# Performance work log

Measured on AMD Instinct MI355X. Metric: run time of the kernel, lower is better.

The kernel has to match this reference:

```python
import jax, jax.numpy as jnp
import numpy as np
from jax import lax

HEADS = 6      # n_splits // head_ratio
DHEAD = 64     # hidden // n_splits
ALLH = HEADS * DHEAD  # 384
KS = 9         # conv_kernel_size
PAD = (KS - 1) // 2


def setup_inputs() -> dict:
    key = jax.random.key(0)
    ks = jax.random.split(key, 12)
    B, S, H = 8, 1024, 768
    f = jnp.float32
    return {
        "Q": jax.random.normal(ks[0], (B, S, H), f),
        "K": jax.random.normal(ks[1], (B, S, H), f),
        "V": jax.random.normal(ks[2], (B, S, H), f),
        "Wq": jax.random.normal(ks[3], (H, ALLH), f) * 0.02,
        "Wk": jax.random.normal(ks[4], (H, ALLH), f) * 0.02,
        "Wv": jax.random.normal(ks[5], (H, ALLH), f) * 0.02,
        "dw": jax.random.normal(ks[6], (H, KS), f) * 0.02,        # depthwise conv [C,k]
        "pw": jax.random.normal(ks[7], (ALLH, H), f) * 0.02,      # pointwise conv [out,in]
        "sep_bias": jnp.zeros((ALLH,), f),
        "Wck": jax.random.normal(ks[8], (ALLH, HEADS * KS), f) * 0.02,
        "bck": jnp.zeros((HEADS * KS,), f),
        "Wco": jax.random.normal(ks[9], (H, ALLH), f) * 0.02,
        "bco": jnp.zeros((ALLH,), f),
        "gammas": jnp.zeros((HEADS, 1, 1), f),
        "mask": jnp.ones((B, S), jnp.int32),
    }


def _forward(Q, K, V, Wq, Wk, Wv, dw, pw, sep_bias, Wck, bck, Wco, bco, gammas, mask):
    B, S, H = Q.shape
    q = Q @ Wq  # [B,S,ALLH]
    k = K @ Wk
    v = V @ Wv
    # SeparableConv1D on K: depthwise 'same' conv (groups=H) then 1x1 pointwise + bias
    x = K.transpose(0, 2, 1)  # [B,H,S]
    x = lax.conv_general_dilated(x, dw[:, None, :], (1,), [(PAD, PAD)],
                                 dimension_numbers=("NCH", "OIH", "NCH"),
                                 feature_group_count=H)
    keyconv = jnp.einsum("bcs,oc->bso", x, pw) + sep_bias  # [B,S,ALLH]
    # span-dynamic-conv kernel weights, softmax over kernel taps
    conv_attn = keyconv * q
    kern = (conv_attn @ Wck + bck).reshape(B, S, HEADS, KS)
    kern = jax.nn.softmax(kern, axis=-1)
    # unfold V-projection into local windows and apply per-position kernels
    co = V @ Wco + bco                                   # [B,S,ALLH]
    cop = jnp.pad(co, ((0, 0), (PAD, PAD), (0, 0)))
    win = jnp.stack([cop[:, j:j + S, :] for j in range(KS)], axis=-1)  # [B,S,ALLH,KS]
    win = win.reshape(B, S, HEADS, DHEAD, KS)
    conv_out = jnp.einsum("bshdk,bshk->bshd", win, kern)  # [B,S,HEADS,DHEAD]
    # standard attention scores
    q4 = q.reshape(B, S, HEADS, DHEAD).transpose(0, 2, 1, 3)
    k4 = k.reshape(B, S, HEADS, DHEAD).transpose(0, 2, 1, 3)
    v4 = v.reshape(B, S, HEADS, DHEAD).transpose(0, 2, 1, 3)
    scores = jnp.einsum("bhid,bhjd->bhij", q4, k4) / jnp.sqrt(jnp.float32(DHEAD))
    m = (mask != 0)[:, None, None, :]  # key mask [B,1,1,S]
    # monotonic distance scores (no-grad in original -> stop_gradient)
    sc = lax.stop_gradient(scores)
    p_ = jax.nn.softmax(jnp.where(m, sc, -1e32), axis=-1) * m.astype(sc.dtype)
    cum = jnp.cumsum(p_, axis=-1)
    tot = jnp.sum(p_, axis=-1, keepdims=True)
    idx = jnp.arange(S)
    pos = jnp.abs(idx[None, :] - idx[:, None]).astype(jnp.float32)  # |i-j|
    dist = jnp.sqrt(jnp.clip((tot - cum) * pos, 0.0))
    gamma = -jax.nn.softplus(gammas)[None]  # [1,HEADS,1,1]
    effect = jnp.clip(jnp.exp(dist * gamma), 1e-5, 1e5)
    scores2 = jnp.where(m, scores * effect, -1e8)
    probs = jax.nn.softmax(scores2, axis=-1)  # dropout_p=0 -> identity
    ctx = jnp.einsum("bhij,bhjd->bihd", probs, v4)  # [B,S,HEADS,DHEAD]
    out = jnp.concatenate([ctx, conv_out], axis=2).reshape(B, S, 2 * ALLH)
    return out


def reference(Q, K, V, Wq, Wk, Wv, dw, pw, sep_bias, Wck, bck, Wco, bco, gammas, mask):
    return _forward(Q, K, V, Wq, Wk, Wv, dw, pw, sep_bias, Wck, bck, Wco, bco, gammas, mask)
```

## Files before the change

kernel.cpp:

```cpp
#include <hip/hip_runtime.h>
#include <math.h>

#define BATCH 8
#define SEQ   1024
#define HID   768
#define HEADS 6
#define DHEAD 64
#define ALLH  384
#define KS    9
#define PADC  4
#define MROWS (BATCH*SEQ)

typedef __attribute__((ext_vector_type(8))) short bf16x8;
typedef __attribute__((ext_vector_type(4))) short bf16x4;
typedef __attribute__((ext_vector_type(4))) float f32x4;

__device__ __forceinline__ ushort f2bf(float x) {
    unsigned u = __float_as_uint(x);
    unsigned r = (u + 0x7FFFu + ((u >> 16) & 1u)) >> 16;
    return (ushort)r;
}
__device__ __forceinline__ unsigned pk2(float a, float b) {
    return (unsigned)f2bf(a) | ((unsigned)f2bf(b) << 16);
}
__device__ __forceinline__ float fexp2(float x) {
#if __has_builtin(__builtin_amdgcn_exp2f)
    return __builtin_amdgcn_exp2f(x);
#else
    return exp2f(x);
#endif
}
__device__ __forceinline__ float fsqrt(float x) {
#if __has_builtin(__builtin_amdgcn_sqrtf)
    return __builtin_amdgcn_sqrtf(x);
#else
    return __sqrtf(x);
#endif
}
__device__ __forceinline__ unsigned cvtpk(float a, float b) {
    unsigned r; asm("v_cvt_pk_bf16_f32 %0, %1, %2" : "=v"(r) : "v"(a), "v"(b)); return r;
}

__device__ __forceinline__ void mfma16(f32x4& c4, bf16x4 a, bf16x4 b) {
#if __has_builtin(__builtin_amdgcn_mfma_f32_16x16x16bf16_1k)
    c4 = __builtin_amdgcn_mfma_f32_16x16x16bf16_1k(a, b, c4, 0, 0, 0);
#else
    asm volatile("v_mfma_f32_16x16x16_bf16 %0, %1, %2, %0" : "+v"(c4) : "v"(a), "v"(b));
#endif
}

__global__ __launch_bounds__(256) void dconv_kernel(const float* __restrict__ Kin,
                                                    const float* __restrict__ dw,
                                                    ushort* __restrict__ y) {
    const int t = threadIdx.x;
    const int c4l = t & 63;
    const int sg = t >> 6;
    const int c4 = blockIdx.x * 64 + c4l;
    const int s0 = blockIdx.y * 64 + sg * 16;
    const int b = blockIdx.z;
    const int c = c4 * 4;

    const float* base = Kin + (size_t)b * SEQ * HID + c;
    ushort* ybase = y + (size_t)b * SEQ * HID + c;

    float wv[4][KS];
#pragma unroll
    for (int j = 0; j < 4; ++j)
#pragma unroll
        for (int tt = 0; tt < KS; ++tt) wv[j][tt] = dw[(c + j) * KS + tt];

    float4 win[KS];
#pragma unroll
    for (int tt = 0; tt < KS; ++tt) {
        int sj = s0 - PADC + tt;
        win[tt] = (sj >= 0 && sj < SEQ) ? *reinterpret_cast<const float4*>(base + (size_t)sj * HID)
                                        : float4{0.f, 0.f, 0.f, 0.f};
    }

#pragma unroll
    for (int i = 0; i < 16; ++i) {
        const int s = s0 + i;
        float4 acc = {0.f, 0.f, 0.f, 0.f};
#pragma unroll
        for (int tt = 0; tt < KS; ++tt) {
            acc.x += win[tt].x * wv[0][tt];
            acc.y += win[tt].y * wv[1][tt];
            acc.z += win[tt].z * wv[2][tt];
            acc.w += win[tt].w * wv[3][tt];
        }
        uint2 o;
        o.x = pk2(acc.x, acc.y); o.y = pk2(acc.z, acc.w);
        *reinterpret_cast<uint2*>(ybase + (size_t)s * HID) = o;
#pragma unroll
        for (int tt = 0; tt < KS - 1; ++tt) win[tt] = win[tt + 1];
        int sj = s + 1 + PADC;
        win[KS - 1] = (sj < SEQ) ? *reinterpret_cast<const float4*>(base + (size_t)sj * HID)
                                 : float4{0.f, 0.f, 0.f, 0.f};
    }
}

__global__ __launch_bounds__(256) void wcvt_kernel(const float* __restrict__ W0, const float* __restrict__ W1,
                                                   const float* __restrict__ W2, const float* __restrict__ W3,
                                                   ushort* __restrict__ O0, ushort* __restrict__ O1,
                                                   ushort* __restrict__ O2, ushort* __restrict__ O3) {
    __shared__ float t[32][33];
    int wsel = blockIdx.z;
    const float* W = wsel == 0 ? W0 : wsel == 1 ? W1 : wsel == 2 ? W2 : W3;
    ushort* O = wsel == 0 ? O0 : wsel == 1 ? O1 : wsel == 2 ? O2 : O3;
    int kt = blockIdx.x * 32;
    int nt = blockIdx.y * 32;
    int tx = threadIdx.x & 31, ty = threadIdx.x >> 5;
#pragma unroll
    for (int i = 0; i < 4; ++i)
        t[ty + i * 8][tx] = W[(size_t)(kt + ty + i * 8) * ALLH + nt + tx];
    __syncthreads();
#pragma unroll
    for (int i = 0; i < 4; ++i)
        O[(size_t)(nt + ty + i * 8) * HID + kt + tx] = f2bf(t[tx][ty + i * 8]);
}

__global__ __launch_bounds__(256) void pwcvt_kernel(const float* __restrict__ pw, ushort* __restrict__ pwb) {
    int i = blockIdx.x * 256 + threadIdx.x;
    if (i < ALLH * HID) pwb[i] = f2bf(pw[i]);
}

template <int BMODE, bool HAS_BIAS, bool AF32>
__global__ __launch_bounds__(256) void gemm_mfma(const void* __restrict__ Ap,
                                                 const ushort* __restrict__ Bt,
                                                 const float* __restrict__ bias,
                                                 float* __restrict__ C,
                                                 ushort* __restrict__ Chm) {
    __shared__ __align__(16) ushort As[64 * 64];
    __shared__ __align__(16) ushort Bs[64 * 64];

    const int bid = blockIdx.x;
    const int swz = (bid & 7) * 96 + (bid >> 3);
    const int n0 = (swz % 6) * 64;
    const int m0 = (swz / 6) * 64;

    const int tid = threadIdx.x;
    const int lane = tid & 63;
    const int w = tid >> 6;
    const int g = lane >> 4;
    const int c = lane & 15;

    const ushort* Ab = (const ushort*)Ap;
    const float* Af = (const float*)Ap;

    f32x4 acc[4] = {{0,0,0,0},{0,0,0,0},{0,0,0,0},{0,0,0,0}};

    for (int k0 = 0; k0 < HID; k0 += 64) {
        __syncthreads();
#pragma unroll
        for (int it = 0; it < 2; ++it) {
            int e = tid + it * 256;
            int row = e >> 3;
            int c8 = (e & 7) * 8;
            int boff = row * 128 + ((c8 * 2) ^ ((row & 7) << 4));
            if (AF32) {
                const float4 f0 = *reinterpret_cast<const float4*>(&Af[(size_t)(m0 + row) * HID + k0 + c8]);
                const float4 f1 = *reinterpret_cast<const float4*>(&Af[(size_t)(m0 + row) * HID + k0 + c8 + 4]);
                uint4 p;
                p.x = pk2(f0.x, f0.y); p.y = pk2(f0.z, f0.w);
                p.z = pk2(f1.x, f1.y); p.w = pk2(f1.z, f1.w);
                *reinterpret_cast<uint4*>((char*)As + boff) = p;
            } else {
                const uint4 av = *reinterpret_cast<const uint4*>(&Ab[(size_t)(m0 + row) * HID + k0 + c8]);
                *reinterpret_cast<uint4*>((char*)As + boff) = av;
            }
            const uint4 bv = *reinterpret_cast<const uint4*>(&Bt[(size_t)(n0 + row) * HID + k0 + c8]);
            *reinterpret_cast<uint4*>((char*)Bs + boff) = bv;
        }
        __syncthreads();

        const int arow = w * 16 + c;
        const int asw = (arow & 7) << 4;
        bf16x8 af0 = *reinterpret_cast<const bf16x8*>((char*)As + arow * 128 + ((g * 16) ^ asw));
        bf16x8 af1 = *reinterpret_cast<const bf16x8*>((char*)As + arow * 128 + ((64 + g * 16) ^ asw));
#pragma unroll
        for (int nq = 0; nq < 4; ++nq) {
            const int brow = nq * 16 + c;
            const int bsw = (brow & 7) << 4;
            bf16x8 bf0 = *reinterpret_cast<const bf16x8*>((char*)Bs + brow * 128 + ((g * 16) ^ bsw));
            bf16x8 bf1 = *reinterpret_cast<const bf16x8*>((char*)Bs + brow * 128 + ((64 + g * 16) ^ bsw));
            acc[nq] = __builtin_amdgcn_mfma_f32_16x16x32_bf16(af0, bf0, acc[nq], 0, 0, 0);
            acc[nq] = __builtin_amdgcn_mfma_f32_16x16x32_bf16(af1, bf1, acc[nq], 0, 0, 0);
        }
    }

#pragma unroll
    for (int nq = 0; nq < 4; ++nq) {
        const int n = n0 + nq * 16 + c;
        const float bv = HAS_BIAS ? bias[n] : 0.f;
#pragma unroll
        for (int r = 0; r < 4; ++r) {
            const int m = m0 + w * 16 + g * 4 + r;
            float v = acc[nq][r] + bv;
            if (BMODE == 0 || BMODE == 1) C[(size_t)m * ALLH + n] = v;
            if (BMODE == 1) {
                int bb = m >> 10, s = m & 1023;
                int head = n >> 6, d = n & 63;
                Chm[(((size_t)bb * HEADS + head) * SEQ + s) * 64 + d] = f2bf(v);
            }
            if (BMODE == 2) {
                int bb = m >> 10, s = m & 1023;
                int head = n >> 6, d = n & 63;
                char* tb = (char*)Chm + (((size_t)(bb * HEADS + head) * 16 + (s >> 6)) * 4096) * 2;
                unsigned off = (unsigned)(s & 63) * 128 + (((unsigned)(d * 2)) ^ ((s & 7) << 4));
                *reinterpret_cast<ushort*>(tb + off) = f2bf(v);
            }
        }
    }
}

__global__ __launch_bounds__(256) void gemm_vv(const float* __restrict__ Af,
                                               const ushort* __restrict__ B1t,
                                               const ushort* __restrict__ B2t,
                                               const float* __restrict__ bco,
                                               ushort* __restrict__ vhm,
                                               float* __restrict__ cob) {
    __shared__ __align__(16) ushort As[64 * 64];
    __shared__ __align__(16) ushort B1s[64 * 64];
    __shared__ __align__(16) ushort B2s[64 * 64];

    const int bid = blockIdx.x;
    const int swz = (bid & 7) * 96 + (bid >> 3);
    const int n0 = (swz % 6) * 64;
    const int m0 = (swz / 6) * 64;

    const int tid = threadIdx.x;
    const int lane = tid & 63;
    const int w = tid >> 6;
    const int g = lane >> 4;
    const int c = lane & 15;

    f32x4 acc1[4] = {{0,0,0,0},{0,0,0,0},{0,0,0,0},{0,0,0,0}};
    f32x4 acc2[4] = {{0,0,0,0},{0,0,0,0},{0,0,0,0},{0,0,0,0}};

    for (int k0 = 0; k0 < HID; k0 += 64) {
        __syncthreads();
#pragma unroll
        for (int it = 0; it < 2; ++it) {
            int e = tid + it * 256;
            int row = e >> 3;
            int c8 = (e & 7) * 8;
            int boff = row * 128 + ((c8 * 2) ^ ((row & 7) << 4));
            const float4 f0 = *reinterpret_cast<const float4*>(&Af[(size_t)(m0 + row) * HID + k0 + c8]);
            const float4 f1 = *reinterpret_cast<const float4*>(&Af[(size_t)(m0 + row) * HID + k0 + c8 + 4]);
            uint4 p;
            p.x = pk2(f0.x, f0.y); p.y = pk2(f0.z, f0.w);
            p.z = pk2(f1.x, f1.y); p.w = pk2(f1.z, f1.w);
            *reinterpret_cast<uint4*>((char*)As + boff) = p;
            const uint4 b1v = *reinterpret_cast<const uint4*>(&B1t[(size_t)(n0 + row) * HID + k0 + c8]);
            *reinterpret_cast<uint4*>((char*)B1s + boff) = b1v;
            const uint4 b2v = *reinterpret_cast<const uint4*>(&B2t[(size_t)(n0 + row) * HID + k0 + c8]);
            *reinterpret_cast<uint4*>((char*)B2s + boff) = b2v;
        }
        __syncthreads();

        const int arow = w * 16 + c;
        const int asw = (arow & 7) << 4;
        bf16x8 af0 = *reinterpret_cast<const bf16x8*>((char*)As + arow * 128 + ((g * 16) ^ asw));
        bf16x8 af1 = *reinterpret_cast<const bf16x8*>((char*)As + arow * 128 + ((64 + g * 16) ^ asw));
#pragma unroll
        for (int nq = 0; nq < 4; ++nq) {
            const int brow = nq * 16 + c;
            const int bsw = (brow & 7) << 4;
            bf16x8 v10 = *reinterpret_cast<const bf16x8*>((char*)B1s + brow * 128 + ((g * 16) ^ bsw));
            bf16x8 v11 = *reinterpret_cast<const bf16x8*>((char*)B1s + brow * 128 + ((64 + g * 16) ^ bsw));
            acc1[nq] = __builtin_amdgcn_mfma_f32_16x16x32_bf16(af0, v10, acc1[nq], 0, 0, 0);
            acc1[nq] = __builtin_amdgcn_mfma_f32_16x16x32_bf16(af1, v11, acc1[nq], 0, 0, 0);
            bf16x8 v20 = *reinterpret_cast<const bf16x8*>((char*)B2s + brow * 128 + ((g * 16) ^ bsw));
            bf16x8 v21 = *reinterpret_cast<const bf16x8*>((char*)B2s + brow * 128 + ((64 + g * 16) ^ bsw));
            acc2[nq] = __builtin_amdgcn_mfma_f32_16x16x32_bf16(af0, v20, acc2[nq], 0, 0, 0);
            acc2[nq] = __builtin_amdgcn_mfma_f32_16x16x32_bf16(af1, v21, acc2[nq], 0, 0, 0);
        }
    }

    {
        const int head = n0 >> 6;
        const int bb = m0 >> 10;
        const int st = (m0 & 1023) >> 6;
        char* tb = (char*)vhm + (((size_t)(bb * HEADS + head) * 16 + st) * 4096) * 2;
#pragma unroll
        for (int nq = 0; nq < 4; ++nq) {
            const int d = nq * 16 + c;
            unsigned off = (unsigned)d * 128 + (((unsigned)(32 * w + 8 * g)) ^ ((d & 7) << 4));
            uint2 vv;
            vv.x = pk2(acc1[nq][0], acc1[nq][1]);
            vv.y = pk2(acc1[nq][2], acc1[nq][3]);
            *reinterpret_cast<uint2*>(tb + off) = vv;
        }
    }
#pragma unroll
    for (int nq = 0; nq < 4; ++nq) {
        const int n = n0 + nq * 16 + c;
        const float bv = bco[n];
#pragma unroll
        for (int r = 0; r < 4; ++r) {
            const int m = m0 + w * 16 + g * 4 + r;
            cob[(size_t)m * ALLH + n] = acc2[nq][r] + bv;
        }
    }
}

__global__ __launch_bounds__(256) void spankern_kernel(const float* __restrict__ keyconv,
                                                       const float* __restrict__ q,
                                                       const float* __restrict__ Wck,
                                                       const float* __restrict__ bck,
                                                       float* __restrict__ kern_sm) {
    __shared__ float ca[4][ALLH];
    __shared__ float kv[4][64];
    int row0 = blockIdx.x * 4;
    int tid = threadIdx.x;
    int r = tid >> 6;
    int lane = tid & 63;
    int row = row0 + r;
    for (int e = lane; e < ALLH; e += 64) {
        size_t off = (size_t)row * ALLH + e;
        ca[r][e] = keyconv[off] * q[off];
    }
    __syncthreads();
    float val = 0.f;
    if (lane < HEADS * KS) {
        for (int kidx = 0; kidx < ALLH; ++kidx)
            val += ca[r][kidx] * Wck[kidx * (HEADS * KS) + lane];
        val += bck[lane];
    }
    kv[r][lane] = val;
    __syncthreads();
    if (lane < HEADS) {
        float mx = -INFINITY;
#pragma unroll
        for (int t = 0; t < KS; ++t) mx = fmaxf(mx, kv[r][lane * KS + t]);
        float e[KS];
        float sum = 0.f;
#pragma unroll
        for (int t = 0; t < KS; ++t) {
            e[t] = expf(kv[r][lane * KS + t] - mx);
            sum += e[t];
        }
        float inv = 1.f / sum;
#pragma unroll
        for (int t = 0; t < KS; ++t)
            kern_sm[((size_t)row * HEADS + lane) * KS + t] = e[t] * inv;
    }
}

__global__ __launch_bounds__(256) void convout_kernel(const float* __restrict__ co,
                                                      const float* __restrict__ kern_sm,
                                                      float* __restrict__ out) {
    int idx = blockIdx.x * 256 + threadIdx.x;
    if (idx >= MROWS * (ALLH / 4)) return;
    int c4 = idx % (ALLH / 4);
    int s = (idx / (ALLH / 4)) % SEQ;
    int b = idx / ((ALLH / 4) * SEQ);
    int c = c4 * 4;
    int h = c >> 6;
    const float* ks = &kern_sm[(((size_t)b * SEQ + s) * HEADS + h) * KS];
    float kt[KS];
#pragma unroll
    for (int t = 0; t < KS; ++t) kt[t] = ks[t];
    float4 acc = {0.f, 0.f, 0.f, 0.f};
#pragma unroll
    for (int t = 0; t < KS; ++t) {
        int sj = s + t - PADC;
        if (sj >= 0 && sj < SEQ) {
            const float4 cv = *reinterpret_cast<const float4*>(&co[((size_t)b * SEQ + sj) * ALLH + c]);
            acc.x += cv.x * kt[t];
            acc.y += cv.y * kt[t];
            acc.z += cv.z * kt[t];
            acc.w += cv.w * kt[t];
        }
    }
    *reinterpret_cast<float4*>(&out[((size_t)b * SEQ + s) * (2 * ALLH) + ALLH + c]) = acc;
}

__global__ __launch_bounds__(256) void attn_mfma(const ushort* __restrict__ qh,
                                                 const ushort* __restrict__ kh,
                                                 const ushort* __restrict__ vh,
                                                 const int* __restrict__ mask,
                                                 const float* __restrict__ gammas,
                                                 float* __restrict__ out) {
    __shared__ __align__(16) ushort kbuf[64 * 64];
    __shared__ __align__(16) ushort vbuf[64 * 64];
    __shared__ float s_msk[SEQ];

    const int bid = blockIdx.x;
    const int blk = (bid & 7) * 96 + (bid >> 3);
    const int qt = blk & 15;
    const int h = (blk >> 4) % HEADS;
    const int b = blk / (16 * HEADS);
    const int i0 = qt * 64;
    const int tid = threadIdx.x;
    const int lane = tid & 63;
    const int w = tid >> 6;
    const int g = lane >> 4;
    const int c = lane & 15;

    const float LOG2E = 1.44269504f;
    float g0 = gammas[h];
    float gamma2 = -(fmaxf(g0, 0.f) + log1pf(expf(-fabsf(g0)))) * LOG2E;
    const float SLOG2 = 0.125f * LOG2E;

    const ushort* ktiles = kh + ((size_t)(b * HEADS + h) * 16) * 4096;
    const ushort* vtiles = vh + ((size_t)(b * HEADS + h) * 16) * 4096;
    const ushort* qhb = qh + ((size_t)b * HEADS + h) * SEQ * 64;

    for (int e = tid; e < SEQ; e += 256)
        s_msk[e] = (mask[b * SEQ + e] != 0) ? 1.f : 0.f;

    bf16x8 qf0, qf1;
    {
        const ushort* qrow = qhb + (size_t)(i0 + w * 16 + c) * 64 + g * 8;
        qf0 = *reinterpret_cast<const bf16x8*>(qrow);
        qf1 = *reinterpret_cast<const bf16x8*>(qrow + 32);
    }

    float Tacc = 0.f;
    for (int chk = 0; chk < 16; ++chk) {
        __syncthreads();
        const ushort* ktp = ktiles + chk * 4096;
#pragma unroll
        for (int it = 0; it < 2; ++it) {
            int e16 = (tid + it * 256) * 16;
            *reinterpret_cast<uint4*>((char*)kbuf + e16) =
                *reinterpret_cast<const uint4*>((const char*)ktp + e16);
        }
        __syncthreads();
        const int j0 = chk * 64;
#pragma unroll
        for (int m = 0; m < 4; ++m) {
            f32x4 acc = {0.f, 0.f, 0.f, 0.f};
            int row = m * 16 + c;
            int sw = (row & 7) << 4;
            bf16x8 kf0 = *reinterpret_cast<const bf16x8*>((char*)kbuf + row * 128 + ((g * 16) ^ sw));
            bf16x8 kf1 = *reinterpret_cast<const bf16x8*>((char*)kbuf + row * 128 + ((64 + g * 16) ^ sw));
            acc = __builtin_amdgcn_mfma_f32_16x16x32_bf16(kf0, qf0, acc, 0, 0, 0);
            acc = __builtin_amdgcn_mfma_f32_16x16x32_bf16(kf1, qf1, acc, 0, 0, 0);
#pragma unroll
            for (int r = 0; r < 4; ++r) {
                float mk = s_msk[j0 + m * 16 + g * 4 + r];
                Tacc += mk * fexp2(acc[r] * SLOG2);
            }
        }
    }
    Tacc += __shfl_xor(Tacc, 16, 64);
    Tacc += __shfl_xor(Tacc, 32, 64);
    const float T = Tacc;
    const float invT = (T > 0.f) ? 1.f / T : 0.f;

    f32x4 ctx0 = {0,0,0,0}, ctx1 = {0,0,0,0}, ctx2 = {0,0,0,0}, ctx3 = {0,0,0,0};
    float l2acc = 0.f;
    float base = 0.f;
    const float iq = (float)(i0 + w * 16 + c);
    const unsigned vx = (unsigned)((c & 7) << 4);

    for (int chk = 0; chk < 16; ++chk) {
        __syncthreads();
        const ushort* ktp = ktiles + chk * 4096;
        const ushort* vtp = vtiles + chk * 4096;
#pragma unroll
        for (int it = 0; it < 2; ++it) {
            int e16 = (tid + it * 256) * 16;
            *reinterpret_cast<uint4*>((char*)kbuf + e16) =
                *reinterpret_cast<const uint4*>((const char*)ktp + e16);
            *reinterpret_cast<uint4*>((char*)vbuf + e16) =
                *reinterpret_cast<const uint4*>((const char*)vtp + e16);
        }
        __syncthreads();
        const int j0 = chk * 64;
#pragma unroll
        for (int m = 0; m < 4; ++m) {
            f32x4 acc = {0.f, 0.f, 0.f, 0.f};
            int row = m * 16 + c;
            int sw = (row & 7) << 4;
            bf16x8 kf0 = *reinterpret_cast<const bf16x8*>((char*)kbuf + row * 128 + ((g * 16) ^ sw));
            bf16x8 kf1 = *reinterpret_cast<const bf16x8*>((char*)kbuf + row * 128 + ((64 + g * 16) ^ sw));
            acc = __builtin_amdgcn_mfma_f32_16x16x32_bf16(kf0, qf0, acc, 0, 0, 0);
            acc = __builtin_amdgcn_mfma_f32_16x16x32_bf16(kf1, qf1, acc, 0, 0, 0);

            float sl[4], mk[4], incl[4];
            float li = 0.f;
#pragma unroll
            for (int r = 0; r < 4; ++r) {
                mk[r] = s_msk[j0 + m * 16 + g * 4 + r];
                sl[r] = acc[r] * SLOG2;
                float e = mk[r] * fexp2(sl[r]);
                li += e;
                incl[r] = li;
            }
            float gs = li;
            float up = __shfl_up(gs, 16, 64); if (g >= 1) gs += up;
            up = __shfl_up(gs, 32, 64); if (g >= 2) gs += up;
            float gexcl = gs - li;
            float ttot = __shfl(gs, 48 + c, 64);

            const float dbase = iq - (float)(j0 + m * 16 + g * 4);
            float p2[4];
#pragma unroll
            for (int r = 0; r < 4; ++r) {
                float cum = base + gexcl + incl[r];
                float rem = fmaxf(1.0f - cum * invT, 0.f);
                float pos = fabsf(dbase - (float)r);
                float dist = fsqrt(rem * pos);
                float eff = fmaxf(fexp2(dist * gamma2), 1e-5f);
                p2[r] = mk[r] * fexp2(sl[r] * eff);
                l2acc += p2[r];
            }
            base += ttot;

            union { uint2 u; bf16x4 v; } pu;
            pu.u.x = cvtpk(p2[0], p2[1]);
            pu.u.y = cvtpk(p2[2], p2[3]);
            bf16x4 pa = pu.v;

            const unsigned cb = ((unsigned)(32 * m + 8 * g)) ^ vx;
#pragma unroll
            for (int t = 0; t < 4; ++t) {
                bf16x4 vfrag = *reinterpret_cast<const bf16x4*>((char*)vbuf + (unsigned)(c + 16 * t) * 128 + cb);
                if (t == 0) mfma16(ctx0, pa, vfrag);
                else if (t == 1) mfma16(ctx1, pa, vfrag);
                else if (t == 2) mfma16(ctx2, pa, vfrag);
                else mfma16(ctx3, pa, vfrag);
            }
        }
    }
    l2acc += __shfl_xor(l2acc, 16, 64);
    l2acc += __shfl_xor(l2acc, 32, 64);
    const float invl2 = 1.f / l2acc;

#pragma unroll
    for (int r = 0; r < 4; ++r) {
        float inv_r = __shfl(invl2, g * 4 + r, 64);
        int qrow = i0 + w * 16 + g * 4 + r;
        float* orow = out + ((size_t)b * SEQ + qrow) * (2 * ALLH) + h * DHEAD;
        orow[c +  0] = ctx0[r] * inv_r;
        orow[c + 16] = ctx1[r] * inv_r;
        orow[c + 32] = ctx2[r] * inv_r;
        orow[c + 48] = ctx3[r] * inv_r;
    }
}

extern "C" void kernel_launch(void* const* d_in, const int* in_sizes, int n_in,
                              void* d_out, int out_size, void* d_ws, size_t ws_size,
                              hipStream_t stream) {
    const float* Q = (const float*)d_in[0];
    const float* Kin = (const float*)d_in[1];
    const float* V = (const float*)d_in[2];
    const float* Wq = (const float*)d_in[3];
    const float* Wk = (const float*)d_in[4];
    const float* Wv = (const float*)d_in[5];
    const float* dw = (const float*)d_in[6];
    const float* pw = (const float*)d_in[7];
    const float* sep_bias = (const float*)d_in[8];
    const float* Wck = (const float*)d_in[9];
    const float* bck = (const float*)d_in[10];
    const float* Wco = (const float*)d_in[11];
    const float* bco = (const float*)d_in[12];
    const float* gammas = (const float*)d_in[13];
    const int* mask = (const int*)d_in[14];
    float* out = (float*)d_out;
    float* ws = (float*)d_ws;

    const size_t NP = (size_t)MROWS * ALLH;
    const size_t WSZ = (size_t)ALLH * HID;
    float* qb   = ws;
    float* cob  = qb + NP;
    float* kcb  = cob + NP;
    float* kern = kcb + NP;
    ushort* qh  = (ushort*)(kern + (size_t)MROWS * HEADS * KS);
    ushort* khm = qh + NP;
    ushort* vhm = khm + NP;
    ushort* ybf = vhm + NP;
    ushort* WqT = ybf + (size_t)MROWS * HID;
    ushort* WkT = WqT + WSZ;
    ushort* WvT = WkT + WSZ;
    ushort* WcoT = WvT + WSZ;
    ushort* pwT = WcoT + WSZ;

    dconv_kernel<<<dim3(3, 16, BATCH), 256, 0, stream>>>(Kin, dw, ybf);
    wcvt_kernel<<<dim3(24, 12, 4), 256, 0, stream>>>(Wq, Wk, Wv, Wco, WqT, WkT, WvT, WcoT);
    pwcvt_kernel<<<(ALLH * HID + 255) / 256, 256, 0, stream>>>(pw, pwT);

    gemm_mfma<1, false, true><<<768, 256, 0, stream>>>(Q, WqT, nullptr, qb, qh);
    gemm_mfma<2, false, true><<<768, 256, 0, stream>>>(Kin, WkT, nullptr, nullptr, khm);
    gemm_vv<<<768, 256, 0, stream>>>(V, WvT, WcoT, bco, vhm, cob);
    gemm_mfma<0, true, false><<<768, 256, 0, stream>>>(ybf, pwT, sep_bias, kcb, nullptr);

    spankern_kernel<<<MROWS / 4, 256, 0, stream>>>(kcb, qb, Wck, bck, kern);

    convout_kernel<<<(MROWS * (ALLH / 4) + 255) / 256, 256, 0, stream>>>(cob, kern, out);

    attn_mfma<<<BATCH * HEADS * (SEQ / 64), 256, 0, stream>>>(qh, khm, vhm, mask, gammas, out);
}
```

Before: 232.6 us.

## Merge projection GEMMs into one launch with 128x128 tiles

Replaces the four separate projection GEMM launches (Q, K, V+Wco fused, pointwise) with a single kernel covering five GEMM units. Each block computes a 128x128 tile, so each wave holds a 4x4 grid of MFMA accumulators. This raises arithmetic intensity per LDS load and removes launch gaps between GEMMs. In exchange it loses the shared V-tile reuse that gemm_vv had for the V and Wco products, and it uses more registers, which may lower occupancy.

New measurement: 226.4 us. -2.6%, faster.

```diff
diff --git a/kernel.cpp b/kernel.cpp
--- a/kernel.cpp
+++ b/kernel.cpp
@@ -124,40 +124,60 @@
     if (i < ALLH * HID) pwb[i] = f2bf(pw[i]);
 }
 
-template <int BMODE, bool HAS_BIAS, bool AF32>
-__global__ __launch_bounds__(256) void gemm_mfma(const void* __restrict__ Ap,
-                                                 const ushort* __restrict__ Bt,
-                                                 const float* __restrict__ bias,
-                                                 float* __restrict__ C,
-                                                 ushort* __restrict__ Chm) {
-    __shared__ __align__(16) ushort As[64 * 64];
-    __shared__ __align__(16) ushort Bs[64 * 64];
-
-    const int bid = blockIdx.x;
-    const int swz = (bid & 7) * 96 + (bid >> 3);
-    const int n0 = (swz % 6) * 64;
-    const int m0 = (swz / 6) * 64;
+__global__ __launch_bounds__(256) void gemm_all(const float* __restrict__ Q,
+                                                const float* __restrict__ Kin,
+                                                const float* __restrict__ V,
+                                                const ushort* __restrict__ ybf,
+                                                const ushort* __restrict__ WqT,
+                                                const ushort* __restrict__ WkT,
+                                                const ushort* __restrict__ WvT,
+                                                const ushort* __restrict__ WcoT,
+                                                const ushort* __restrict__ pwT,
+                                                const float* __restrict__ bco,
+                                                const float* __restrict__ sep_bias,
+                                                float* __restrict__ qb,
+                                                ushort* __restrict__ qh,
+                                                ushort* __restrict__ khm,
+                                                ushort* __restrict__ vhm,
+                                                float* __restrict__ cob,
+                                                float* __restrict__ kcb) {
+    __shared__ __align__(16) ushort As[128 * 64];
+    __shared__ __align__(16) ushort Bs[128 * 64];
+
+    const int bx = blockIdx.x;
+    const int swz = (bx & 7) * 120 + (bx >> 3);
+    const int unit = swz / 192;
+    const int local = swz % 192;
+    const int n0 = (local % 3) * 128;
+    const int m0 = (local / 3) * 128;
+
+    const float* Af = unit == 0 ? Q : unit == 1 ? Kin : V;
+    const ushort* Ab = ybf;
+    const ushort* Bt = unit == 0 ? WqT : unit == 1 ? WkT : unit == 2 ? WvT : unit == 3 ? WcoT : pwT;
+    const bool af32 = (unit != 4);
 
     const int tid = threadIdx.x;
     const int lane = tid & 63;
     const int w = tid >> 6;
+    const int wr = w >> 1, wc = w & 1;
     const int g = lane >> 4;
     const int c = lane & 15;
 
-    const ushort* Ab = (const ushort*)Ap;
-    const float* Af = (const float*)Ap;
-
-    f32x4 acc[4] = {{0,0,0,0},{0,0,0,0},{0,0,0,0},{0,0,0,0}};
+    f32x4 acc[4][4];
+#pragma unroll
+    for (int i = 0; i < 4; ++i)
+#pragma unroll
+        for (int j = 0; j < 4; ++j) acc[i][j] = f32x4{0.f, 0.f, 0.f, 0.f};
 
     for (int k0 = 0; k0 < HID; k0 += 64) {
         __syncthreads();
 #pragma unroll
-        for (int it = 0; it < 2; ++it) {
+        for (int it = 0; it < 4; ++it) {
             int e = tid + it * 256;
             int row = e >> 3;
             int c8 = (e & 7) * 8;
             int boff = row * 128 + ((c8 * 2) ^ ((row & 7) << 4));
-            if (AF32) {
+            if (af32) {
                 const float4 f0 = *reinterpret_cast<const float4*>(&Af[(size_t)(m0 + row) * HID + k0 + c8]);
                 const float4 f1 = *reinterpret_cast<const float4*>(&Af[(size_t)(m0 + row) * HID + k0 + c8 + 4]);
                 uint4 p;
@@ -173,133 +193,80 @@
         }
         __syncthreads();
 
-        const int arow = w * 16 + c;
-        const int asw = (arow & 7) << 4;
-        bf16x8 af0 = *reinterpret_cast<const bf16x8*>((char*)As + arow * 128 + ((g * 16) ^ asw));
-        bf16x8 af1 = *reinterpret_cast<const bf16x8*>((char*)As + arow * 128 + ((64 + g * 16) ^ asw));
+        bf16x8 af0[4], af1[4];
+#pragma unroll
+        for (int mq = 0; mq < 4; ++mq) {
+            const int arow = wr * 64 + mq * 16 + c;
+            const int asw = (arow & 7) << 4;
+            af0[mq] = *reinterpret_cast<const bf16x8*>((char*)As + arow * 128 + ((g * 16) ^ asw));
+            af1[mq] = *reinterpret_cast<const bf16x8*>((char*)As + arow * 128 + ((64 + g * 16) ^ asw));
+        }
 #pragma unroll
         for (int nq = 0; nq < 4; ++nq) {
-            const int brow = nq * 16 + c;
+            const int brow = wc * 64 + nq * 16 + c;
             const int bsw = (brow & 7) << 4;
             bf16x8 bf0 = *reinterpret_cast<const bf16x8*>((char*)Bs + brow * 128 + ((g * 16) ^ bsw));
             bf16x8 bf1 = *reinterpret_cast<const bf16x8*>((char*)Bs + brow * 128 + ((64 + g * 16) ^ bsw));
-            acc[nq] = __builtin_amdgcn_mfma_f32_16x16x32_bf16(af0, bf0, acc[nq], 0, 0, 0);
-            acc[nq] = __builtin_amdgcn_mfma_f32_16x16x32_bf16(af1, bf1, acc[nq], 0, 0, 0);
-        }
+#pragma unroll
+            for (int mq = 0; mq < 4; ++mq) {
+                acc[mq][nq] = __builtin_amdgcn_mfma_f32_16x16x32_bf16(af0[mq], bf0, acc[mq][nq], 0, 0, 0);
+                acc[mq][nq] = __builtin_amdgcn_mfma_f32_16x16x32_bf16(af1[mq], bf1, acc[mq][nq], 0, 0, 0);
+            }
+        }
+    }
+
+    if (unit == 2) {
+#pragma unroll
+        for (int mq = 0; mq < 4; ++mq) {
+            const int mbase = m0 + wr * 64 + mq * 16 + g * 4;
+            const int bb = mbase >> 10;
+            const int st = (mbase & 1023) >> 6;
+            const unsigned colb = (unsigned)(32 * mq + 8 * g);
+#pragma unroll
+            for (int nq = 0; nq < 4; ++nq) {
+                const int n = n0 + wc * 64 + nq * 16 + c;
+                const int head = n >> 6;
+                const int d = n & 63;
+                char* tb = (char*)vhm + (((size_t)(bb * HEADS + head) * 16 + st) * 4096) * 2;
+                unsigned off = (unsigned)d * 128 + (colb ^ ((d & 7) << 4));
+                uint2 vv;
+                vv.x = pk2(acc[mq][nq][0], acc[mq][nq][1]);
+                vv.y = pk2(acc[mq][nq][2], acc[mq][nq][3]);
+                *reinterpret_cast<uint2*>(tb + off) = vv;
+            }
+        }
+        return;
     }
 
 #pragma unroll
     for (int nq = 0; nq < 4; ++nq) {
-        const int n = n0 + nq * 16 + c;
-        const float bv = HAS_BIAS ? bias[n] : 0.f;
-#pragma unroll
-        for (int r = 0; r < 4; ++r) {
-            const int m = m0 + w * 16 + g * 4 + r;
-            float v = acc[nq][r] + bv;
-            if (BMODE == 0 || BMODE == 1) C[(size_t)m * ALLH + n] = v;
-            if (BMODE == 1) {
-                int bb = m >> 10, s = m & 1023;
-                int head = n >> 6, d = n & 63;
-                Chm[(((size_t)bb * HEADS + head) * SEQ + s) * 64 + d] = f2bf(v);
-            }
-            if (BMODE == 2) {
-                int bb = m >> 10, s = m & 1023;
-                int head = n >> 6, d = n & 63;
-                char* tb = (char*)Chm + (((size_t)(bb * HEADS + head) * 16 + (s >> 6)) * 4096) * 2;
-                unsigned off = (unsigned)(s & 63) * 128 + (((unsigned)(d * 2)) ^ ((s & 7) << 4));
-                *reinterpret_cast<ushort*>(tb + off) = f2bf(v);
-            }
-        }
-    }
-}
-
-__global__ __launch_bounds__(256) void gemm_vv(const float* __restrict__ Af,
-                                               const ushort* __restrict__ B1t,
-                                               const ushort* __restrict__ B2t,
-                                               const float* __restrict__ bco,
-                                               ushort* __restrict__ vhm,
-                                               float* __restrict__ cob) {
-    __shared__ __align__(16) ushort As[64 * 64];
-    __shared__ __align__(16) ushort B1s[64 * 64];
-    __shared__ __align__(16) ushort B2s[64 * 64];
-
-    const int bid = blockIdx.x;
-    const int swz = (bid & 7) * 96 + (bid >> 3);
-    const int n0 = (swz % 6) * 64;
-    const int m0 = (swz / 6) * 64;
-
-    const int tid = threadIdx.x;
-    const int lane = tid & 63;
-    const int w = tid >> 6;
-    const int g = lane >> 4;
-    const int c = lane & 15;
-
-    f32x4 acc1[4] = {{0,0,0,0},{0,0,0,0},{0,0,0,0},{0,0,0,0}};
-    f32x4 acc2[4] = {{0,0,0,0},{0,0,0,0},{0,0,0,0},{0,0,0,0}};
-
-    for (int k0 = 0; k0 < HID; k0 += 64) {
-        __syncthreads();
-#pragma unroll
-        for (int it = 0; it < 2; ++it) {
-            int e = tid + it * 256;
-            int row = e >> 3;
-            int c8 = (e & 7) * 8;
-            int boff = row * 128 + ((c8 * 2) ^ ((row & 7) << 4));
-            const float4 f0 = *reinterpret_cast<const float4*>(&Af[(size_t)(m0 + row) * HID + k0 + c8]);
-            const float4 f1 = *reinterpret_cast<const float4*>(&Af[(size_t)(m0 + row) * HID + k0 + c8 + 4]);
-            uint4 p;
-            p.x = pk2(f0.x, f0.y); p.y = pk2(f0.z, f0.w);
-            p.z = pk2(f1.x, f1.y); p.w = pk2(f1.z, f1.w);
-            *reinterpret_cast<uint4*>((char*)As + boff) = p;
-            const uint4 b1v = *reinterpret_cast<const uint4*>(&B1t[(size_t)(n0 + row) * HID + k0 + c8]);
-            *reinterpret_cast<uint4*>((char*)B1s + boff) = b1v;
-            const uint4 b2v = *reinterpret_cast<const uint4*>(&B2t[(size_t)(n0 + row) * HID + k0 + c8]);
-            *reinterpret_cast<uint4*>((char*)B2s + boff) = b2v;
-        }
-        __syncthreads();
-
-        const int arow = w * 16 + c;
-        const int asw = (arow & 7) << 4;
-        bf16x8 af0 = *reinterpret_cast<const bf16x8*>((char*)As + arow * 128 + ((g * 16) ^ asw));
-        bf16x8 af1 = *reinterpret_cast<const bf16x8*>((char*)As + arow * 128 + ((64 + g * 16) ^ asw));
-#pragma unroll
-        for (int nq = 0; nq < 4; ++nq) {
-            const int brow = nq * 16 + c;
-            const int bsw = (brow & 7) << 4;
-            bf16x8 v10 = *reinterpret_cast<const bf16x8*>((char*)B1s + brow * 128 + ((g * 16) ^ bsw));
-            bf16x8 v11 = *reinterpret_cast<const bf16x8*>((char*)B1s + brow * 128 + ((64 + g * 16) ^ bsw));
-            acc1[nq] = __builtin_amdgcn_mfma_f32_16x16x32_bf16(af0, v10, acc1[nq], 0, 0, 0);
-            acc1[nq] = __builtin_amdgcn_mfma_f32_16x16x32_bf16(af1, v11, acc1[nq], 0, 0, 0);
-            bf16x8 v20 = *reinterpret_cast<const bf16x8*>((char*)B2s + brow * 128 + ((g * 16) ^ bsw));
-            bf16x8 v21 = *reinterpret_cast<const bf16x8*>((char*)B2s + brow * 128 + ((64 + g * 16) ^ bsw));
-            acc2[nq] = __builtin_amdgcn_mfma_f32_16x16x32_bf16(af0, v20, acc2[nq], 0, 0, 0);
-            acc2[nq] = __builtin_amdgcn_mfma_f32_16x16x32_bf16(af1, v21, acc2[nq], 0, 0, 0);
-        }
-    }
-
-    {
-        const int head = n0 >> 6;
-        const int bb = m0 >> 10;
-        const int st = (m0 & 1023) >> 6;
-        char* tb = (char*)vhm + (((size_t)(bb * HEADS + head) * 16 + st) * 4096) * 2;
-#pragma unroll
-        for (int nq = 0; nq < 4; ++nq) {
-            const int d = nq * 16 + c;
-            unsigned off = (unsigned)d * 128 + (((unsigned)(32 * w + 8 * g)) ^ ((d & 7) << 4));
-            uint2 vv;
-            vv.x = pk2(acc1[nq][0], acc1[nq][1]);
-            vv.y = pk2(acc1[nq][2], acc1[nq][3]);
-            *reinterpret_cast<uint2*>(tb + off) = vv;
-        }
-    }
-#pragma unroll
-    for (int nq = 0; nq < 4; ++nq) {
-        const int n = n0 + nq * 16 + c;
-        const float bv = bco[n];
-#pragma unroll
-        for (int r = 0; r < 4; ++r) {
-            const int m = m0 + w * 16 + g * 4 + r;
-            cob[(size_t)m * ALLH + n] = acc2[nq][r] + bv;
+        const int n = n0 + wc * 64 + nq * 16 + c;
+        float bv = 0.f;
+        if (unit == 3) bv = bco[n];
+        if (unit == 4) bv = sep_bias[n];
+#pragma unroll
+        for (int mq = 0; mq < 4; ++mq) {
+#pragma unroll
+            for (int r = 0; r < 4; ++r) {
+                const int m = m0 + wr * 64 + mq * 16 + g * 4 + r;
+                float v = acc[mq][nq][r] + bv;
+                if (unit == 0) {
+                    qb[(size_t)m * ALLH + n] = v;
+                    int bb = m >> 10, s = m & 1023;
+                    int head = n >> 6, d = n & 63;
+                    qh[(((size_t)bb * HEADS + head) * SEQ + s) * 64 + d] = f2bf(v);
+                } else if (unit == 1) {
+                    int bb = m >> 10, s = m & 1023;
+                    int head = n >> 6, d = n & 63;
+                    char* tb = (char*)khm + (((size_t)(bb * HEADS + head) * 16 + (s >> 6)) * 4096) * 2;
+                    unsigned off = (unsigned)(s & 63) * 128 + (((unsigned)(d * 2)) ^ ((s & 7) << 4));
+                    *reinterpret_cast<ushort*>(tb + off) = f2bf(v);
+                } else if (unit == 3) {
+                    cob[(size_t)m * ALLH + n] = v;
+                } else {
+                    kcb[(size_t)m * ALLH + n] = v;
+                }
+            }
         }
     }
 }
@@ -583,10 +550,8 @@
     wcvt_kernel<<<dim3(24, 12, 4), 256, 0, stream>>>(Wq, Wk, Wv, Wco, WqT, WkT, WvT, WcoT);
     pwcvt_kernel<<<(ALLH * HID + 255) / 256, 256, 0, stream>>>(pw, pwT);
 
-    gemm_mfma<1, false, true><<<768, 256, 0, stream>>>(Q, WqT, nullptr, qb, qh);
-    gemm_mfma<2, false, true><<<768, 256, 0, stream>>>(Kin, WkT, nullptr, nullptr, khm);
-    gemm_vv<<<768, 256, 0, stream>>>(V, WvT, WcoT, bco, vhm, cob);
-    gemm_mfma<0, true, false><<<768, 256, 0, stream>>>(ybf, pwT, sep_bias, kcb, nullptr);
+    gemm_all<<<960, 256, 0, stream>>>(Q, Kin, V, ybf, WqT, WkT, WvT, WcoT, pwT,
+                                      bco, sep_bias, qb, qh, khm, vhm, cob, kcb);
 
     spankern_kernel<<<MROWS / 4, 256, 0, stream>>>(kcb, qb, Wck, bck, kern);
 
```
